# Optimization experiments

Hardware: AMD Instinct MI355X
Metric: run time of the kernel (lower is better)

## Reference

```python
import jax, jax.numpy as jnp
import numpy as np

PAD_IDX = 0  # tgt_dict.stoi[PAD_WORD]
TLEN, BATCH, SLEN, CVOCAB = 64, 32, 128, 64
D, VOCAB = 1024, 50257


def setup_inputs() -> dict:
    key = jax.random.key(0)
    ks = jax.random.split(key, 7)
    hidden = jax.random.normal(ks[0], (TLEN * BATCH, D), dtype=jnp.float32)
    # attention distribution over source positions (rows sum to 1)
    attn = jax.nn.softmax(jax.random.normal(ks[1], (TLEN * BATCH, SLEN), dtype=jnp.float32), axis=-1)
    # sparse one-hot indicator: each source position maps to one extended-vocab slot
    src_idx = jax.random.randint(ks[2], (SLEN, BATCH), 0, CVOCAB)
    src_map = jax.nn.one_hot(src_idx, CVOCAB, dtype=jnp.float32)  # [slen, batch, cvocab]
    W_gen = jax.random.normal(ks[3], (VOCAB, D), dtype=jnp.float32) * 0.02
    b_gen = jnp.zeros((VOCAB,), dtype=jnp.float32)
    W_copy = jax.random.normal(ks[4], (1, D), dtype=jnp.float32) * 0.02
    b_copy = jnp.zeros((1,), dtype=jnp.float32)
    return {"hidden": hidden, "attn": attn, "src_map": src_map,
            "W_gen": W_gen, "b_gen": b_gen, "W_copy": W_copy, "b_copy": b_copy}


def reference(hidden, attn, src_map, W_gen, b_gen, W_copy, b_copy):
    slen, batch, cvocab = src_map.shape
    # p_softmax over tgt dict, with PAD masked to -inf before softmax
    logits = hidden @ W_gen.T + b_gen                      # [N, vocab]
    logits = logits.at[:, PAD_IDX].set(-jnp.inf)
    prob = jax.nn.softmax(logits, axis=-1)                 # [N, vocab]
    # copy gate p(z)
    p_copy = jax.nn.sigmoid(hidden @ W_copy.T + b_copy)    # [N, 1]
    out_prob = prob * (1.0 - p_copy)                       # [N, vocab]
    mul_attn = attn * p_copy                               # [N, slen]
    # torch flattening is tlen-major: view(-1, batch, slen) -> [tlen, batch, slen]
    mul_attn = mul_attn.reshape(-1, batch, slen)
    # bmm against sparse one-hot indicator: [tlen,batch,slen] x [slen,batch,cvocab]
    copy_prob = jnp.einsum('tbs,sbc->tbc', mul_attn, src_map)
    copy_prob = copy_prob.reshape(-1, cvocab)              # [N, cvocab]
    return jnp.concatenate([out_prob, copy_prob], axis=1)  # [N, vocab+cvocab]
```

## Files before the change

kernel.cpp:

```cpp
#include <hip/hip_runtime.h>
#include <hip/hip_bf16.h>

#define VOCAB 50257
#define CVOCAB 64
#define OUTW (VOCAB + CVOCAB)
#define DDIM 1024
#define NROWS 2048
#define SLEN 128
#define NVT 393
#define NVT2 197
#define VOCABP2 (NVT2 * 256)
#define RSTRIDE 72

typedef __attribute__((ext_vector_type(8))) short bf16x8;
typedef __attribute__((ext_vector_type(4))) float f32x4;
typedef __attribute__((ext_vector_type(2))) unsigned long long u64x2;

__device__ __forceinline__ unsigned short f2bf(float f) {
  union { float f; unsigned u; } x; x.f = f;
  unsigned r = x.u + 0x7FFFu + ((x.u >> 16) & 1u);
  return (unsigned short)(r >> 16);
}

__device__ __forceinline__ unsigned char f2e4m3(float f) {
  unsigned u = __float_as_uint(f);
  unsigned s = (u >> 24) & 0x80u;
  float a = __uint_as_float(u & 0x7FFFFFFFu);
  if (!(a < 448.f)) a = 448.f;
  if (a < 0.015625f) {
    int q = (int)rintf(a * 512.f);
    return (unsigned char)(s | (unsigned)q);
  }
  unsigned b = __float_as_uint(a);
  unsigned lsb = (b >> 20) & 1u;
  b += 0x0007FFFFu + lsb;
  int e = (int)((b >> 23) & 0xFF) - 127;
  unsigned m = (b >> 20) & 7u;
  return (unsigned char)(s | ((unsigned)(e + 7) << 3) | m);
}

__device__ __forceinline__ unsigned pack_e4m3x4(float a, float b, float c, float d) {
#if __has_builtin(__builtin_amdgcn_cvt_pk_fp8_f32)
  int r = __builtin_amdgcn_cvt_pk_fp8_f32(a, b, 0, false);
  r = __builtin_amdgcn_cvt_pk_fp8_f32(c, d, r, true);
  return (unsigned)r;
#else
  return (unsigned)f2e4m3(a) | ((unsigned)f2e4m3(b) << 8) |
         ((unsigned)f2e4m3(c) << 16) | ((unsigned)f2e4m3(d) << 24);
#endif
}

__global__ __launch_bounds__(256) void k_pcopy(const float* __restrict__ hidden,
                                               const float* __restrict__ Wc,
                                               const float* __restrict__ bc,
                                               float* __restrict__ pc) {
  int n = blockIdx.x * 4 + (threadIdx.x >> 6);
  int lane = threadIdx.x & 63;
  const float4* h = (const float4*)(hidden + (size_t)n * DDIM);
  const float4* w = (const float4*)Wc;
  float s = 0.0f;
  for (int i = lane; i < DDIM / 4; i += 64) {
    float4 a = h[i], b = w[i];
    s += a.x * b.x + a.y * b.y + a.z * b.z + a.w * b.w;
  }
  #pragma unroll
  for (int m = 1; m < 64; m <<= 1) s += __shfl_xor(s, m);
  if (lane == 0) pc[n] = 1.0f / (1.0f + __expf(-(s + bc[0])));
}

__global__ __launch_bounds__(256) void k_cvtA8(const float* __restrict__ src,
                                               unsigned char* __restrict__ dst) {
  int i = blockIdx.x * 256 + threadIdx.x;
  float4 v = *(const float4*)(src + (size_t)i * 4);
  *(unsigned*)(dst + (size_t)i * 4) = pack_e4m3x4(v.x, v.y, v.z, v.w);
}

__global__ __launch_bounds__(256) void k_cvtW8(const float* __restrict__ Wg,
                                               unsigned char* __restrict__ Wf8) {
  int row = blockIdx.x;
  int t = threadIdx.x;
  unsigned r = 0;
  if (row < VOCAB) {
    float4 v = *(const float4*)(Wg + (size_t)row * DDIM + t * 4);
    r = pack_e4m3x4(v.x * 64.f, v.y * 64.f, v.z * 64.f, v.w * 64.f);
  }
  *(unsigned*)(Wf8 + (size_t)row * DDIM + t * 4) = r;
}

template<int OM>
__global__ __launch_bounds__(512, 2) void k_gemm8(const unsigned char* __restrict__ A,
                                                  const unsigned char* __restrict__ W,
                                                  const float* __restrict__ bg,
                                                  float* __restrict__ out,
                                                  unsigned short* __restrict__ ebuf,
                                                  float* __restrict__ partial) {
  __shared__ __align__(16) unsigned char sA[2][256 * RSTRIDE];
  __shared__ __align__(16) unsigned char sB[2][256 * RSTRIDE];
  __shared__ float psum[1024];

  const int tid = threadIdx.x;
  const int lane = tid & 63;
  const int w = tid >> 6;
  const int wr = w >> 2, wn = w & 3;
  const int lrow = lane & 15, kgrp = lane >> 4;

  int swz = (blockIdx.x & 7) * 197 + (blockIdx.x >> 3);
  const int mt = swz & 7, vt = swz >> 3;
  const int m0 = mt * 256;
  const int v0 = vt * 256;

  const int srow = tid >> 2, scol = (tid & 3) * 16;
  const size_t gA0 = (size_t)(m0 + srow) * DDIM + scol;
  const size_t gA1 = gA0 + (size_t)128 * DDIM;
  const size_t gW0 = (size_t)(v0 + srow) * DDIM + scol;
  const size_t gW1 = gW0 + (size_t)128 * DDIM;
  const int l0 = srow * RSTRIDE + scol;
  const int l1 = l0 + 128 * RSTRIDE;

  int aoff[8], boff[4];
  #pragma unroll
  for (int rf = 0; rf < 8; rf++)
    aoff[rf] = (wr * 128 + rf * 16 + lrow) * RSTRIDE + kgrp * 8;
  #pragma unroll
  for (int cf = 0; cf < 4; cf++)
    boff[cf] = (wn * 64 + cf * 16 + lrow) * RSTRIDE + kgrp * 8;

  f32x4 acc[8][4] = {};

  u64x2 ra0, ra1, rb0, rb1;

  #define LOADT(t) { \
    ra0 = *(const u64x2*)(A + gA0 + (t) * 64); \
    ra1 = *(const u64x2*)(A + gA1 + (t) * 64); \
    rb0 = *(const u64x2*)(W + gW0 + (t) * 64); \
    rb1 = *(const u64x2*)(W + gW1 + (t) * 64); \
  }
  #define WRITET(buf) { \
    unsigned char* da = &sA[buf][0]; \
    unsigned char* db = &sB[buf][0]; \
    *(unsigned long long*)(da + l0)     = ra0[0]; \
    *(unsigned long long*)(da + l0 + 8) = ra0[1]; \
    *(unsigned long long*)(da + l1)     = ra1[0]; \
    *(unsigned long long*)(da + l1 + 8) = ra1[1]; \
    *(unsigned long long*)(db + l0)     = rb0[0]; \
    *(unsigned long long*)(db + l0 + 8) = rb0[1]; \
    *(unsigned long long*)(db + l1)     = rb1[0]; \
    *(unsigned long long*)(db + l1 + 8) = rb1[1]; \
  }

  LOADT(0);
  WRITET(0);
  asm volatile("s_waitcnt lgkmcnt(0)" ::: "memory");
  __builtin_amdgcn_s_barrier();

  for (int t = 0; t < 16; t++) {
    const unsigned char* pa = &sA[t & 1][0];
    const unsigned char* pb = &sB[t & 1][0];
    unsigned long long a0[8], b0[4];
    #pragma unroll
    for (int rf = 0; rf < 8; rf++) a0[rf] = *(const unsigned long long*)(pa + aoff[rf]);
    #pragma unroll
    for (int cf = 0; cf < 4; cf++) b0[cf] = *(const unsigned long long*)(pb + boff[cf]);
    if (t < 15) LOADT(t + 1);
    __builtin_amdgcn_s_setprio(1);
    #pragma unroll
    for (int rf = 0; rf < 8; rf++)
      #pragma unroll
      for (int cf = 0; cf < 4; cf++)
        acc[rf][cf] = __builtin_amdgcn_mfma_f32_16x16x32_fp8_fp8(
            (long)a0[rf], (long)b0[cf], acc[rf][cf], 0, 0, 0);
    __builtin_amdgcn_s_setprio(0);
    unsigned long long a1[8], b1[4];
    #pragma unroll
    for (int rf = 0; rf < 8; rf++) a1[rf] = *(const unsigned long long*)(pa + aoff[rf] + 32);
    #pragma unroll
    for (int cf = 0; cf < 4; cf++) b1[cf] = *(const unsigned long long*)(pb + boff[cf] + 32);
    __builtin_amdgcn_s_setprio(1);
    #pragma unroll
    for (int rf = 0; rf < 8; rf++)
      #pragma unroll
      for (int cf = 0; cf < 4; cf++)
        acc[rf][cf] = __builtin_amdgcn_mfma_f32_16x16x32_fp8_fp8(
            (long)a1[rf], (long)b1[cf], acc[rf][cf], 0, 0, 0);
    __builtin_amdgcn_s_setprio(0);
    if (t < 15) WRITET((t + 1) & 1);
    asm volatile("s_waitcnt lgkmcnt(0)" ::: "memory");
    __builtin_amdgcn_s_barrier();
  }
  #undef LOADT
  #undef WRITET

  const float INV = 0.015625f;
  float bgv[4];
  int vcol[4];
  #pragma unroll
  for (int cf = 0; cf < 4; cf++) {
    vcol[cf] = v0 + wn * 64 + cf * 16 + lrow;
    bgv[cf] = (vcol[cf] < VOCAB) ? bg[vcol[cf]] : 0.0f;
  }
  #pragma unroll
  for (int a = 0; a < 8; a++) {
    #pragma unroll
    for (int r = 0; r < 4; r++) {
      int lr = wr * 128 + a * 16 + kgrp * 4 + r;
      int row = m0 + lr;
      float s = 0.0f;
      #pragma unroll
      for (int cf = 0; cf < 4; cf++) {
        int v = vcol[cf];
        float e = 0.0f;
        if (v < VOCAB && v != 0) e = __expf(acc[a][cf][r] * INV + bgv[cf]);
        if (OM == 0) {
          if (v < VOCAB) out[(size_t)row * OUTW + v] = e;
        } else {
          if (v < VOCAB) ebuf[(size_t)row * VOCABP2 + v + (row & 3)] = f2bf(e);
        }
        s += e;
      }
      s += __shfl_xor(s, 1); s += __shfl_xor(s, 2);
      s += __shfl_xor(s, 4); s += __shfl_xor(s, 8);
      if (lrow == 0) psum[wn * 256 + lr] = s;
    }
  }
  __syncthreads();
  if (tid < 256)
    partial[(size_t)vt * NROWS + m0 + tid] =
        psum[tid] + psum[256 + tid] + psum[512 + tid] + psum[768 + tid];
}

__global__ __launch_bounds__(256) void k_gemm(const float* __restrict__ hidden,
                                              const float* __restrict__ Wg,
                                              const float* __restrict__ bg,
                                              float* __restrict__ out,
                                              float* __restrict__ partial) {
  __shared__ __align__(16) unsigned char smemA[128 * 64 * 2];
  __shared__ __align__(16) unsigned char smemB[128 * 64 * 2];
  __shared__ float psum[2][128];

  const int tid = threadIdx.x;
  const int lane = tid & 63;
  const int wid = tid >> 6;
  const int wr = wid >> 1, wc = wid & 1;
  const int lrow = lane & 15, kgrp = lane >> 4;
  const int m0 = blockIdx.x * 128;
  const int vt = blockIdx.y;
  const int v0 = vt * 128;

  f32x4 acc[4][4] = {};

  for (int kt = 0; kt < 16; kt++) {
    const int k0 = kt * 64;
    #pragma unroll
    for (int i = 0; i < 8; i++) {
      int f = i * 256 + tid;
      int row = f >> 4;
      int kq = (f & 15) << 2;
      float4 v = *(const float4*)(hidden + (size_t)(m0 + row) * DDIM + k0 + kq);
      ushort4 h;
      h.x = f2bf(v.x); h.y = f2bf(v.y); h.z = f2bf(v.z); h.w = f2bf(v.w);
      *(ushort4*)(smemA + row * 128 + ((kq << 1) ^ ((row & 7) << 4))) = h;
    }
    #pragma unroll
    for (int i = 0; i < 8; i++) {
      int f = i * 256 + tid;
      int row = f >> 4;
      int kq = (f & 15) << 2;
      float4 v = make_float4(0.f, 0.f, 0.f, 0.f);
      if (v0 + row < VOCAB)
        v = *(const float4*)(Wg + (size_t)(v0 + row) * DDIM + k0 + kq);
      ushort4 h;
      h.x = f2bf(v.x); h.y = f2bf(v.y); h.z = f2bf(v.z); h.w = f2bf(v.w);
      *(ushort4*)(smemB + row * 128 + ((kq << 1) ^ ((row & 7) << 4))) = h;
    }
    __syncthreads();
    #pragma unroll
    for (int ks = 0; ks < 2; ks++) {
      const int kb = (ks * 32 + kgrp * 8) * 2;
      bf16x8 af[4], bfr[4];
      #pragma unroll
      for (int i = 0; i < 4; i++) {
        int ar = wr * 64 + i * 16 + lrow;
        af[i] = *(const bf16x8*)(smemA + ar * 128 + (kb ^ ((ar & 7) << 4)));
        int br = wc * 64 + i * 16 + lrow;
        bfr[i] = *(const bf16x8*)(smemB + br * 128 + (kb ^ ((br & 7) << 4)));
      }
      #pragma unroll
      for (int i = 0; i < 4; i++)
        #pragma unroll
        for (int j = 0; j < 4; j++)
          acc[i][j] = __builtin_amdgcn_mfma_f32_16x16x32_bf16(af[i], bfr[j], acc[i][j], 0, 0, 0);
    }
    __syncthreads();
  }

  float bgv[4];
  int vcol[4];
  #pragma unroll
  for (int j = 0; j < 4; j++) {
    vcol[j] = v0 + wc * 64 + j * 16 + lrow;
    bgv[j] = (vcol[j] < VOCAB) ? bg[vcol[j]] : 0.0f;
  }
  #pragma unroll
  for (int i = 0; i < 4; i++) {
    #pragma unroll
    for (int r = 0; r < 4; r++) {
      int row = m0 + wr * 64 + i * 16 + kgrp * 4 + r;
      float s = 0.0f;
      #pragma unroll
      for (int j = 0; j < 4; j++) {
        int v = vcol[j];
        float e = 0.0f;
        if (v < VOCAB && v != 0) e = __expf(acc[i][j][r] + bgv[j]);
        if (v < VOCAB) out[(size_t)row * OUTW + v] = e;
        s += e;
      }
      s += __shfl_xor(s, 1); s += __shfl_xor(s, 2);
      s += __shfl_xor(s, 4); s += __shfl_xor(s, 8);
      if ((lane & 15) == 0) psum[wc][wr * 64 + i * 16 + kgrp * 4 + r] = s;
    }
  }
  __syncthreads();
  if (tid < 128)
    partial[(size_t)vt * NROWS + m0 + tid] = psum[0][tid] + psum[1][tid];
}

__global__ __launch_bounds__(256) void k_reduce(const float* __restrict__ partial,
                                                const float* __restrict__ pc,
                                                float* __restrict__ scale, int nvt) {
  int n = blockIdx.x * 256 + threadIdx.x;
  float s = 0.0f;
  for (int t = 0; t < nvt; t++) s += partial[(size_t)t * NROWS + n];
  scale[n] = (1.0f - pc[n]) / s;
}

__global__ __launch_bounds__(256) void k_scale(float* __restrict__ out,
                                               const float* __restrict__ scale) {
  int n = blockIdx.x;
  float sc = scale[n];
  size_t base = (size_t)n * OUTW;
  int off = (int)((4 - (base & 3)) & 3);
  for (int c = threadIdx.x; c < off; c += 256) out[base + c] *= sc;
  int nv = (VOCAB - off) >> 2;
  f32x4* p = (f32x4*)(out + base + off);
  for (int i = threadIdx.x; i < nv; i += 256) {
    f32x4 v = p[i];
    v *= sc;
    __builtin_nontemporal_store(v, &p[i]);
  }
  for (int c = off + (nv << 2) + threadIdx.x; c < VOCAB; c += 256) out[base + c] *= sc;
}

__global__ __launch_bounds__(256) void k_scale2(const unsigned short* __restrict__ ebuf,
                                                const float* __restrict__ scale,
                                                float* __restrict__ out) {
  int n = blockIdx.x;
  float sc = scale[n];
  const int shift = n & 3;
  const int off = (4 - shift) & 3;
  const unsigned short* er = ebuf + (size_t)n * VOCABP2 + shift;
  float* orow = out + (size_t)n * OUTW;
  for (int c = threadIdx.x; c < off; c += 256)
    orow[c] = __uint_as_float((unsigned)er[c] << 16) * sc;
  int nv = (VOCAB - off) >> 2;
  for (int i = threadIdx.x; i < nv; i += 256) {
    int c = off + i * 4;
    ushort4 v = *(const ushort4*)(er + c);
    f32x4 f;
    f.x = __uint_as_float((unsigned)v.x << 16) * sc;
    f.y = __uint_as_float((unsigned)v.y << 16) * sc;
    f.z = __uint_as_float((unsigned)v.z << 16) * sc;
    f.w = __uint_as_float((unsigned)v.w << 16) * sc;
    __builtin_nontemporal_store(f, (f32x4*)(orow + c));
  }
  for (int c = off + (nv << 2) + threadIdx.x; c < VOCAB; c += 256)
    orow[c] = __uint_as_float((unsigned)er[c] << 16) * sc;
}

__global__ __launch_bounds__(64) void k_copy(const float* __restrict__ attn,
                                             const float* __restrict__ src_map,
                                             const float* __restrict__ pc,
                                             float* __restrict__ out) {
  int n = blockIdx.x;
  int c = threadIdx.x;
  int b = n & 31;
  __shared__ float arow[SLEN];
  arow[c] = attn[(size_t)n * SLEN + c];
  arow[c + 64] = attn[(size_t)n * SLEN + 64 + c];
  __syncthreads();
  float s = 0.0f;
  for (int sp = 0; sp < SLEN; sp++)
    s += arow[sp] * src_map[((size_t)sp * 32 + b) * CVOCAB + c];
  out[(size_t)n * OUTW + VOCAB + c] = s * pc[n];
}

extern "C" void kernel_launch(void* const* d_in, const int* in_sizes, int n_in,
                              void* d_out, int out_size, void* d_ws, size_t ws_size,
                              hipStream_t stream) {
  const float* hidden = (const float*)d_in[0];
  const float* attn   = (const float*)d_in[1];
  const float* srcmap = (const float*)d_in[2];
  const float* Wg     = (const float*)d_in[3];
  const float* bg     = (const float*)d_in[4];
  const float* Wc     = (const float*)d_in[5];
  const float* bc     = (const float*)d_in[6];
  float* out = (float*)d_out;

  char* ws = (char*)d_ws;
  float* pc      = (float*)ws;
  float* scale   = (float*)(ws + 8192);
  float* partial = (float*)(ws + 16384);
  size_t partEnd = 16384 + (size_t)NVT * NROWS * 4;
  unsigned char* A8 = (unsigned char*)(ws + partEnd);
  size_t aEnd = partEnd + (size_t)NROWS * DDIM;
  unsigned char* W8 = (unsigned char*)(ws + aEnd);
  size_t wEnd = aEnd + (size_t)VOCABP2 * DDIM;
  unsigned short* ebuf = (unsigned short*)(ws + wEnd);
  size_t need1 = wEnd;
  size_t need2 = wEnd + (size_t)NROWS * VOCABP2 * 2;

  k_pcopy<<<NROWS / 4, 256, 0, stream>>>(hidden, Wc, bc, pc);
  if (ws_size >= need1) {
    k_cvtA8<<<(NROWS * DDIM / 4) / 256, 256, 0, stream>>>(hidden, A8);
    k_cvtW8<<<VOCABP2, 256, 0, stream>>>(Wg, W8);
    if (ws_size >= need2) {
      k_gemm8<1><<<8 * NVT2, 512, 0, stream>>>(A8, W8, bg, out, ebuf, partial);
      k_reduce<<<NROWS / 256, 256, 0, stream>>>(partial, pc, scale, NVT2);
      k_scale2<<<NROWS, 256, 0, stream>>>(ebuf, scale, out);
    } else {
      k_gemm8<0><<<8 * NVT2, 512, 0, stream>>>(A8, W8, bg, out, ebuf, partial);
      k_reduce<<<NROWS / 256, 256, 0, stream>>>(partial, pc, scale, NVT2);
      k_scale<<<NROWS, 256, 0, stream>>>(out, scale);
    }
  } else {
    k_gemm<<<dim3(NROWS / 128, NVT), 256, 0, stream>>>(hidden, Wg, bg, out, partial);
    k_reduce<<<NROWS / 256, 256, 0, stream>>>(partial, pc, scale, NVT);
    k_scale<<<NROWS, 256, 0, stream>>>(out, scale);
  }
  k_copy<<<NROWS, 64, 0, stream>>>(attn, srcmap, pc, out);
}
```

Baseline: 463.6 us.

## Use MX-scaled 16x16x128 FP8 MFMA over paired K-tiles and parallelize row reduce

Restructures the FP8 GEMM main loop to process two 64-wide K tiles per iteration and, when available, issue the gfx950 scaled 16x16x128 f8f6f4 MFMA with unit scales instead of four 16x16x32 FP8 MFMAs. This cuts the MFMA instruction count and may raise matrix throughput, at the cost of more live registers and an extra barrier per tile pair. The reduce kernel is also changed from one thread per row to 32 lanes per row with a shuffle reduction, to spread the strided partial-sum reads across more threads.

Result: faster. 410.0 us (-11.6%).

```diff
diff --git a/kernel.cpp b/kernel.cpp
--- a/kernel.cpp
+++ b/kernel.cpp
@@ -15,6 +15,13 @@
 typedef __attribute__((ext_vector_type(8))) short bf16x8;
 typedef __attribute__((ext_vector_type(4))) float f32x4;
 typedef __attribute__((ext_vector_type(2))) unsigned long long u64x2;
+typedef __attribute__((ext_vector_type(8))) int i32x8;
+
+#if __has_builtin(__builtin_amdgcn_mfma_scale_f32_16x16x128_f8f6f4)
+#define MXOK 1
+#else
+#define MXOK 0
+#endif
 
 __device__ __forceinline__ unsigned short f2bf(float f) {
   union { float f; unsigned u; } x; x.f = f;
@@ -48,6 +55,16 @@
   return (unsigned)f2e4m3(a) | ((unsigned)f2e4m3(b) << 8) |
          ((unsigned)f2e4m3(c) << 16) | ((unsigned)f2e4m3(d) << 24);
 #endif
+}
+
+__device__ __forceinline__ i32x8 mk8(unsigned long long x0, unsigned long long x1,
+                                     unsigned long long x2, unsigned long long x3) {
+  i32x8 r;
+  r[0] = (int)x0; r[1] = (int)(x0 >> 32);
+  r[2] = (int)x1; r[3] = (int)(x1 >> 32);
+  r[4] = (int)x2; r[5] = (int)(x2 >> 32);
+  r[6] = (int)x3; r[7] = (int)(x3 >> 32);
+  return r;
 }
 
 __global__ __launch_bounds__(256) void k_pcopy(const float* __restrict__ hidden,
@@ -128,6 +145,7 @@
   f32x4 acc[8][4] = {};
 
   u64x2 ra0, ra1, rb0, rb1;
+  unsigned long long ae0[8], ae1[8], be0[4], be1[4];
 
   #define LOADT(t) { \
     ra0 = *(const u64x2*)(A + gA0 + (t) * 64); \
@@ -153,39 +171,79 @@
   asm volatile("s_waitcnt lgkmcnt(0)" ::: "memory");
   __builtin_amdgcn_s_barrier();
 
-  for (int t = 0; t < 16; t++) {
-    const unsigned char* pa = &sA[t & 1][0];
-    const unsigned char* pb = &sB[t & 1][0];
-    unsigned long long a0[8], b0[4];
-    #pragma unroll
-    for (int rf = 0; rf < 8; rf++) a0[rf] = *(const unsigned long long*)(pa + aoff[rf]);
-    #pragma unroll
-    for (int cf = 0; cf < 4; cf++) b0[cf] = *(const unsigned long long*)(pb + boff[cf]);
-    if (t < 15) LOADT(t + 1);
-    __builtin_amdgcn_s_setprio(1);
-    #pragma unroll
-    for (int rf = 0; rf < 8; rf++)
+  for (int tp = 0; tp < 8; tp++) {
+    const int t = tp * 2;
+    {
+      const unsigned char* pa = &sA[0][0];
+      const unsigned char* pb = &sB[0][0];
+      #pragma unroll
+      for (int rf = 0; rf < 8; rf++) {
+        ae0[rf] = *(const unsigned long long*)(pa + aoff[rf]);
+        ae1[rf] = *(const unsigned long long*)(pa + aoff[rf] + 32);
+      }
+      #pragma unroll
+      for (int cf = 0; cf < 4; cf++) {
+        be0[cf] = *(const unsigned long long*)(pb + boff[cf]);
+        be1[cf] = *(const unsigned long long*)(pb + boff[cf] + 32);
+      }
+      LOADT(t + 1);
+      WRITET(1);
+      asm volatile("s_waitcnt lgkmcnt(0)" ::: "memory");
+      __builtin_amdgcn_s_barrier();
+    }
+    {
+      const unsigned char* pa = &sA[1][0];
+      const unsigned char* pb = &sB[1][0];
+      unsigned long long ao0[8], ao1[8], bo0[4], bo1[4];
+      #pragma unroll
+      for (int rf = 0; rf < 8; rf++) {
+        ao0[rf] = *(const unsigned long long*)(pa + aoff[rf]);
+        ao1[rf] = *(const unsigned long long*)(pa + aoff[rf] + 32);
+      }
+      #pragma unroll
+      for (int cf = 0; cf < 4; cf++) {
+        bo0[cf] = *(const unsigned long long*)(pb + boff[cf]);
+        bo1[cf] = *(const unsigned long long*)(pb + boff[cf] + 32);
+      }
+      const bool pf = (tp < 7);
+      if (pf) LOADT(t + 2);
+      __builtin_amdgcn_s_setprio(1);
+#if MXOK
+      i32x8 bfr[4];
       #pragma unroll
       for (int cf = 0; cf < 4; cf++)
-        acc[rf][cf] = __builtin_amdgcn_mfma_f32_16x16x32_fp8_fp8(
-            (long)a0[rf], (long)b0[cf], acc[rf][cf], 0, 0, 0);
-    __builtin_amdgcn_s_setprio(0);
-    unsigned long long a1[8], b1[4];
-    #pragma unroll
-    for (int rf = 0; rf < 8; rf++) a1[rf] = *(const unsigned long long*)(pa + aoff[rf] + 32);
-    #pragma unroll
-    for (int cf = 0; cf < 4; cf++) b1[cf] = *(const unsigned long long*)(pb + boff[cf] + 32);
-    __builtin_amdgcn_s_setprio(1);
-    #pragma unroll
-    for (int rf = 0; rf < 8; rf++)
-      #pragma unroll
-      for (int cf = 0; cf < 4; cf++)
-        acc[rf][cf] = __builtin_amdgcn_mfma_f32_16x16x32_fp8_fp8(
-            (long)a1[rf], (long)b1[cf], acc[rf][cf], 0, 0, 0);
-    __builtin_amdgcn_s_setprio(0);
-    if (t < 15) WRITET((t + 1) & 1);
-    asm volatile("s_waitcnt lgkmcnt(0)" ::: "memory");
-    __builtin_amdgcn_s_barrier();
+        bfr[cf] = mk8(be0[cf], be1[cf], bo0[cf], bo1[cf]);
+      #pragma unroll
+      for (int rf = 0; rf < 8; rf++) {
+        i32x8 afr = mk8(ae0[rf], ae1[rf], ao0[rf], ao1[rf]);
+        #pragma unroll
+        for (int cf = 0; cf < 4; cf++)
+          acc[rf][cf] = __builtin_amdgcn_mfma_scale_f32_16x16x128_f8f6f4(
+              afr, bfr[cf], acc[rf][cf], 0, 0,
+              0, 0x7F7F7F7F, 0, 0x7F7F7F7F);
+      }
+#else
+      #pragma unroll
+      for (int rf = 0; rf < 8; rf++)
+        #pragma unroll
+        for (int cf = 0; cf < 4; cf++) {
+          acc[rf][cf] = __builtin_amdgcn_mfma_f32_16x16x32_fp8_fp8(
+              (long)ae0[rf], (long)be0[cf], acc[rf][cf], 0, 0, 0);
+          acc[rf][cf] = __builtin_amdgcn_mfma_f32_16x16x32_fp8_fp8(
+              (long)ae1[rf], (long)be1[cf], acc[rf][cf], 0, 0, 0);
+          acc[rf][cf] = __builtin_amdgcn_mfma_f32_16x16x32_fp8_fp8(
+              (long)ao0[rf], (long)bo0[cf], acc[rf][cf], 0, 0, 0);
+          acc[rf][cf] = __builtin_amdgcn_mfma_f32_16x16x32_fp8_fp8(
+              (long)ao1[rf], (long)bo1[cf], acc[rf][cf], 0, 0, 0);
+        }
+#endif
+      __builtin_amdgcn_s_setprio(0);
+      if (pf) {
+        WRITET(0);
+        asm volatile("s_waitcnt lgkmcnt(0)" ::: "memory");
+        __builtin_amdgcn_s_barrier();
+      }
+    }
   }
   #undef LOADT
   #undef WRITET
@@ -327,10 +385,13 @@
 __global__ __launch_bounds__(256) void k_reduce(const float* __restrict__ partial,
                                                 const float* __restrict__ pc,
                                                 float* __restrict__ scale, int nvt) {
-  int n = blockIdx.x * 256 + threadIdx.x;
+  int row = blockIdx.x * 8 + (threadIdx.x >> 5);
+  int sl = threadIdx.x & 31;
   float s = 0.0f;
-  for (int t = 0; t < nvt; t++) s += partial[(size_t)t * NROWS + n];
-  scale[n] = (1.0f - pc[n]) / s;
+  for (int t = sl; t < nvt; t += 32) s += partial[(size_t)t * NROWS + row];
+  s += __shfl_xor(s, 1); s += __shfl_xor(s, 2); s += __shfl_xor(s, 4);
+  s += __shfl_xor(s, 8); s += __shfl_xor(s, 16);
+  if (sl == 0) scale[row] = (1.0f - pc[row]) / s;
 }
 
 __global__ __launch_bounds__(256) void k_scale(float* __restrict__ out,
@@ -424,16 +485,16 @@
     k_cvtW8<<<VOCABP2, 256, 0, stream>>>(Wg, W8);
     if (ws_size >= need2) {
       k_gemm8<1><<<8 * NVT2, 512, 0, stream>>>(A8, W8, bg, out, ebuf, partial);
-      k_reduce<<<NROWS / 256, 256, 0, stream>>>(partial, pc, scale, NVT2);
+      k_reduce<<<NROWS / 8, 256, 0, stream>>>(partial, pc, scale, NVT2);
       k_scale2<<<NROWS, 256, 0, stream>>>(ebuf, scale, out);
     } else {
       k_gemm8<0><<<8 * NVT2, 512, 0, stream>>>(A8, W8, bg, out, ebuf, partial);
-      k_reduce<<<NROWS / 256, 256, 0, stream>>>(partial, pc, scale, NVT2);
+      k_reduce<<<NROWS / 8, 256, 0, stream>>>(partial, pc, scale, NVT2);
       k_scale<<<NROWS, 256, 0, stream>>>(out, scale);
     }
   } else {
     k_gemm<<<dim3(NROWS / 128, NVT), 256, 0, stream>>>(hidden, Wg, bg, out, partial);
-    k_reduce<<<NROWS / 256, 256, 0, stream>>>(partial, pc, scale, NVT);
+    k_reduce<<<NROWS / 8, 256, 0, stream>>>(partial, pc, scale, NVT);
     k_scale<<<NROWS, 256, 0, stream>>>(out, scale);
   }
   k_copy<<<NROWS, 64, 0, stream>>>(attn, srcmap, pc, out);
```
